# Performance work log

Hardware: AMD Instinct MI355X
Metric: run time of the kernel (lower is better)

## Reference

```python
import jax, jax.numpy as jnp
import numpy as np

N = 50000
E = 800000
DIN = 128
HID = 128
H = 4
C = HID // H  # 32
NEG_SLOPE = 0.2


def _lin(k, fin, fout):
    return jax.random.normal(k, (fin, fout), jnp.float32) * (1.0 / np.sqrt(fin))


def setup_inputs() -> dict:
    key = jax.random.key(0)
    ks = jax.random.split(key, 24)
    x = jax.random.normal(ks[0], (N, DIN), jnp.float32)
    src = jax.random.randint(ks[1], (E,), 0, N)
    dst = (src + jax.random.randint(ks[2], (E,), 1, N)) % N  # no self-loops
    edge_index = jnp.stack([src, dst]).astype(jnp.int32)
    edge_weight = jax.random.uniform(ks[3], (E,), jnp.float32)
    p = {}
    for i, koff in ((0, 4), (1, 12)):
        fin = DIN if i == 0 else HID
        p[f"Wl{i}"] = _lin(ks[koff + 0], fin, HID)
        p[f"bl{i}"] = jnp.zeros((HID,), jnp.float32)
        p[f"Wr{i}"] = _lin(ks[koff + 1], fin, HID)
        p[f"br{i}"] = jnp.zeros((HID,), jnp.float32)
        p[f"We{i}"] = _lin(ks[koff + 2], 1, HID)
        p[f"att{i}"] = jax.random.normal(ks[koff + 3], (H, C), jnp.float32) * (1.0 / np.sqrt(C))
        p[f"b{i}"] = jnp.zeros((HID,), jnp.float32)
    p["prelu_a"] = jnp.float32(0.25)
    return dict(x=x, edge_index=edge_index, edge_weight=edge_weight, **p)


def gatv2_layer(x, src, dst, ea, Wl, bl, Wr, br, We, att, bias):
    n = x.shape[0]
    # self-loop edge_attr = per-dst mean of incoming edge_attr (fill_value='mean')
    deg = jax.ops.segment_sum(jnp.ones((ea.shape[0],), ea.dtype), dst, num_segments=n)
    loop_ea = jax.ops.segment_sum(ea, dst, num_segments=n) / jnp.maximum(deg, 1.0)[:, None]
    loops = jnp.arange(n, dtype=src.dtype)
    srcf = jnp.concatenate([src, loops])
    dstf = jnp.concatenate([dst, loops])
    eaf = jnp.concatenate([ea, loop_ea], axis=0)
    xl = (x @ Wl + bl).reshape(n, H, C)  # source transform (lin_l)
    xr = (x @ Wr + br).reshape(n, H, C)  # target transform (lin_r)
    eproj = (eaf @ We).reshape(-1, H, C)  # lin_edge, bias=False
    m = xl[srcf] + xr[dstf] + eproj  # [E+N, H, C]
    s = jnp.where(m >= 0, m, NEG_SLOPE * m)  # LeakyReLU(0.2)
    logits = jnp.einsum("ehc,hc->eh", s, att)
    # segment softmax over dst
    lmax = jax.lax.stop_gradient(jax.ops.segment_max(logits, dstf, num_segments=n))
    a = jnp.exp(logits - lmax[dstf])
    denom = jax.ops.segment_sum(a, dstf, num_segments=n)
    a = a / denom[dstf]
    out = jax.ops.segment_sum(a[:, :, None] * xl[srcf], dstf, num_segments=n)
    return out.reshape(n, H * C) + bias


def reference(x, edge_index, edge_weight,
              Wl0, bl0, Wr0, br0, We0, att0, b0,
              Wl1, bl1, Wr1, br1, We1, att1, b1,
              prelu_a):
    src, dst = edge_index[0], edge_index[1]
    ea = edge_weight[:, None]  # [E, 1]
    h = gatv2_layer(x, src, dst, ea, Wl0, bl0, Wr0, br0, We0, att0, b0)
    h = jnp.where(h >= 0, h, prelu_a * h)  # PReLU (dropout=0 -> identity)
    h = gatv2_layer(h, src, dst, ea, Wl1, bl1, Wr1, br1, We1, att1, b1)
    return h
```

## Files before the change

kernel.cpp:

```cpp
#include <hip/hip_runtime.h>
#include <hip/hip_bf16.h>
#include <math.h>

#define NN 50000
#define NE 800000
#define HD 128
#define MNEG (-1e30f)
#define LOG2E 1.44269504088896340736f

typedef __attribute__((ext_vector_type(8))) short short8;
typedef __attribute__((ext_vector_type(16))) float f32x16;

__global__ void k_edge_count(const int* __restrict__ ei,
                             int* __restrict__ deg, int* __restrict__ rank) {
    int e = blockIdx.x * blockDim.x + threadIdx.x;
    if (e >= NE) return;
    int d = ei[NE + e];
    rank[e] = atomicAdd(&deg[d], 1);
}

__global__ void k_scan1(const int* __restrict__ deg, int* __restrict__ offs,
                        int* __restrict__ bsums) {
    __shared__ int sh[256];
    int t = threadIdx.x;
    int i = blockIdx.x * 256 + t;
    int v = (i < NN) ? deg[i] : 0;
    sh[t] = v;
    __syncthreads();
    for (int off = 1; off < 256; off <<= 1) {
        int x = (t >= off) ? sh[t - off] : 0;
        __syncthreads();
        sh[t] += x;
        __syncthreads();
    }
    if (i < NN) offs[i] = sh[t] - v;
    if (t == 255) bsums[blockIdx.x] = sh[255];
}

__global__ void k_scan2(int* __restrict__ bsums, int nb) {
    __shared__ int sh[256];
    int t = threadIdx.x;
    int v = (t < nb) ? bsums[t] : 0;
    sh[t] = v;
    __syncthreads();
    for (int off = 1; off < 256; off <<= 1) {
        int x = (t >= off) ? sh[t - off] : 0;
        __syncthreads();
        sh[t] += x;
        __syncthreads();
    }
    if (t < nb) bsums[t] = sh[t] - v;
}

__global__ void k_scan3(int* __restrict__ offs, const int* __restrict__ bsums) {
    int i = blockIdx.x * 256 + threadIdx.x;
    if (i == 0) offs[NN] = NE;
    if (i >= NN) return;
    offs[i] += bsums[blockIdx.x];
}

__global__ void k_csr_fill(const int* __restrict__ ei, const float* __restrict__ ew,
                           const int* __restrict__ rank, const int* __restrict__ offs,
                           int2* __restrict__ csr) {
    int e = blockIdx.x * blockDim.x + threadIdx.x;
    if (e >= NE) return;
    int d = ei[NE + e];
    csr[offs[d] + rank[e]] = make_int2(ei[e], __float_as_int(ew[e]));
}

__device__ __forceinline__ void f2bf2(float x, short& h, short& l) {
    __hip_bfloat16 hb = __float2bfloat16(x);
    float hf = __bfloat162float(hb);
    __hip_bfloat16 lb = __float2bfloat16(x - hf);
    h = *reinterpret_cast<short*>(&hb);
    l = *reinterpret_cast<short*>(&lb);
}

__device__ __forceinline__ void load8(const float* __restrict__ p, float* r) {
    float4 t0 = *(const float4*)p;
    float4 t1 = *(const float4*)(p + 4);
    r[0] = t0.x; r[1] = t0.y; r[2] = t0.z; r[3] = t0.w;
    r[4] = t1.x; r[5] = t1.y; r[6] = t1.z; r[7] = t1.w;
}

__global__ void k_pack(const float* __restrict__ Wl, const float* __restrict__ Wr,
                       short* __restrict__ bhi, short* __restrict__ blo) {
    int idx = blockIdx.x * blockDim.x + threadIdx.x;
    if (idx >= 8 * 8 * 64 * 8) return;
    int j = idx & 7;
    int lane = (idx >> 3) & 63;
    int q = (idx >> 9) & 7;
    int t = idx >> 12;
    int col = t * 32 + (lane & 31);
    int k = q * 16 + ((lane >> 5) << 3) + j;
    float v = (col < 128) ? Wl[k * 128 + col] : Wr[k * 128 + (col - 128)];
    short h, l;
    f2bf2(v, h, l);
    bhi[idx] = h;
    blo[idx] = l;
}

template <bool AF32>
__global__ __launch_bounds__(256, 3) void k_gemm_mfma(
        const float* __restrict__ Af,
        const short* __restrict__ Ahi, const short* __restrict__ Alo,
        const short* __restrict__ Bhi, const short* __restrict__ Blo,
        const float* __restrict__ bl, const float* __restrict__ br,
        float* __restrict__ outl, float* __restrict__ outr) {
    int ch = blockIdx.x & 1;
    int rowblk = blockIdx.x >> 1;
    int lane = threadIdx.x & 63;
    int m0 = rowblk * 128 + (threadIdx.x >> 6) * 32;
    if (m0 >= NN) return;

    int arow = m0 + (lane & 31);
    size_t abase = (size_t)(arow < NN ? arow : 0) * HD + ((lane >> 5) << 3);

    f32x16 acc[4];
#pragma unroll
    for (int t = 0; t < 4; ++t)
#pragma unroll
        for (int r = 0; r < 16; ++r) acc[t][r] = 0.f;

    const short8* Bh8 = (const short8*)Bhi;
    const short8* Bl8 = (const short8*)Blo;

#pragma unroll
    for (int q = 0; q < 8; ++q) {
        short8 ah, al;
        if constexpr (AF32) {
            float vv[8];
            load8(&Af[abase + q * 16], vv);
#pragma unroll
            for (int k2 = 0; k2 < 8; ++k2) {
                short h, l;
                f2bf2(vv[k2], h, l);
                ah[k2] = h;
                al[k2] = l;
            }
        } else {
            ah = *(const short8*)(Ahi + abase + q * 16);
            al = *(const short8*)(Alo + abase + q * 16);
        }
#pragma unroll
        for (int t2 = 0; t2 < 4; ++t2) {
            int t = ch * 4 + t2;
            short8 bh = Bh8[(t * 8 + q) * 64 + lane];
            short8 bl_ = Bl8[(t * 8 + q) * 64 + lane];
            acc[t2] = __builtin_amdgcn_mfma_f32_32x32x16_bf16(ah, bh, acc[t2], 0, 0, 0);
            acc[t2] = __builtin_amdgcn_mfma_f32_32x32x16_bf16(al, bh, acc[t2], 0, 0, 0);
            acc[t2] = __builtin_amdgcn_mfma_f32_32x32x16_bf16(ah, bl_, acc[t2], 0, 0, 0);
        }
    }

    int colr = lane & 31;
    int rowoff = (lane >> 5) << 2;
#pragma unroll
    for (int t2 = 0; t2 < 4; ++t2) {
        int colg = (ch * 4 + t2) * 32 + colr;
        float bias = (colg < 128) ? bl[colg] : br[colg - 128];
        float* dst = (colg < 128) ? (outl + colg) : (outr + (colg - 128));
#pragma unroll
        for (int r = 0; r < 16; ++r) {
            int rw = m0 + (r & 3) + ((r >> 2) << 3) + rowoff;
            if (rw < NN) dst[(size_t)rw * HD] = acc[t2][r] + bias;
        }
    }
}


__device__ __forceinline__ float dotpart(const float* xv, const float* xrv,
                                         const float* wev, const float* atv, float w) {
    float part = 0.f;
#pragma unroll
    for (int k = 0; k < 8; ++k) {
        float t = fmaf(w, wev[k], xrv[k]) + xv[k];
        t = fmaxf(t, 0.2f * t);
        part = fmaf(atv[k], t, part);
    }
    part += __shfl_xor(part, 1);
    part += __shfl_xor(part, 2);
    return part;
}

__device__ __forceinline__ void upd(float part, const float* xv,
                                    float& m, float& s, float* o) {
    float newm = fmaxf(m, part);
    float sc = exp2f(m - newm);
    float p = exp2f(part - newm);
    s = fmaf(s, sc, p);
#pragma unroll
    for (int k = 0; k < 8; ++k) o[k] = fmaf(o[k], sc, p * xv[k]);
    m = newm;
}

template <bool PRELU, bool OUTBF>
__global__ __launch_bounds__(256) void k_node(
        const float* __restrict__ xl, const float* __restrict__ xr,
        const int* __restrict__ offs, const int2* __restrict__ csr,
        const float* __restrict__ We, const float* __restrict__ att,
        const float* __restrict__ bias, const float* __restrict__ prelu,
        float* __restrict__ out, short* __restrict__ ohi, short* __restrict__ olo) {
    int wid = (blockIdx.x * blockDim.x + threadIdx.x) >> 6;
    if (wid >= NN) return;
    const int lane = threadIdx.x & 63;
    const int g = lane >> 4;
    const int j = lane & 15;
    const int c0 = j << 3;
    const int v = wid;

    float xrv[8], wev[8], atv[8];
    load8(&xr[(size_t)v * HD + c0], xrv);
    load8(&We[c0], wev);
    load8(&att[c0], atv);
#pragma unroll
    for (int k = 0; k < 8; ++k) atv[k] *= LOG2E;

    const int beg = offs[v];
    const int deg = offs[v + 1] - beg;

    float mA = MNEG, sA = 0.f, mB = MNEG, sB = 0.f, wsum = 0.f;
    float oA[8], oB[8];
#pragma unroll
    for (int k = 0; k < 8; ++k) { oA[k] = 0.f; oB[k] = 0.f; }

    int i = g;
    for (; i + 4 < deg; i += 8) {
        int2 e0 = csr[beg + i];
        int2 e1 = csr[beg + i + 4];
        float w0 = __int_as_float(e0.y), w1 = __int_as_float(e1.y);
        float xv0[8], xv1[8];
        load8(&xl[(size_t)e0.x * HD + c0], xv0);
        load8(&xl[(size_t)e1.x * HD + c0], xv1);
        float p0 = dotpart(xv0, xrv, wev, atv, w0);
        float p1 = dotpart(xv1, xrv, wev, atv, w1);
        upd(p0, xv0, mA, sA, oA);
        upd(p1, xv1, mB, sB, oB);
        wsum += w0 + w1;
    }
    if (i < deg) {
        int2 e0 = csr[beg + i];
        float w0 = __int_as_float(e0.y);
        float xv0[8];
        load8(&xl[(size_t)e0.x * HD + c0], xv0);
        float p0 = dotpart(xv0, xrv, wev, atv, w0);
        upd(p0, xv0, mA, sA, oA);
        wsum += w0;
    }

    float m, s, o[8];
    {
        m = fmaxf(mA, mB);
        float a = exp2f(mA - m), b = exp2f(mB - m);
        s = sA * a + sB * b;
#pragma unroll
        for (int k = 0; k < 8; ++k) o[k] = oA[k] * a + oB[k] * b;
    }

#pragma unroll
    for (int d = 16; d < 64; d <<= 1) {
        float m2 = __shfl_xor(m, d);
        float s2 = __shfl_xor(s, d);
        wsum += __shfl_xor(wsum, d);
        float M = fmaxf(m, m2);
        float a = exp2f(m - M), b = exp2f(m2 - M);
        s = s * a + s2 * b;
#pragma unroll
        for (int k = 0; k < 8; ++k) {
            float o2 = __shfl_xor(o[k], d);
            o[k] = o[k] * a + o2 * b;
        }
        m = M;
    }

    {
        float wself = wsum / fmaxf((float)deg, 1.f);
        float xv[8];
        load8(&xl[(size_t)v * HD + c0], xv);
        float part = dotpart(xv, xrv, wev, atv, wself);
        float newm = fmaxf(m, part);
        float a = exp2f(m - newm), p = exp2f(part - newm);
        s = s * a + p;
#pragma unroll
        for (int k = 0; k < 8; ++k) o[k] = fmaf(o[k], a, p * xv[k]);
    }

    if (g == 0) {
        float bi[8];
        load8(&bias[c0], bi);
        float inv = 1.f / s;
        float r[8];
#pragma unroll
        for (int k = 0; k < 8; ++k) r[k] = fmaf(o[k], inv, bi[k]);
        if (PRELU) {
            float a = *prelu;
#pragma unroll
            for (int k = 0; k < 8; ++k) r[k] = (r[k] >= 0.f) ? r[k] : a * r[k];
        }
        if (OUTBF) {
            short8 h8, l8;
#pragma unroll
            for (int k = 0; k < 8; ++k) {
                short h, l;
                f2bf2(r[k], h, l);
                h8[k] = h;
                l8[k] = l;
            }
            *(short8*)&ohi[(size_t)v * HD + c0] = h8;
            *(short8*)&olo[(size_t)v * HD + c0] = l8;
        } else {
            float* op = &out[(size_t)v * HD + c0];
            *(float4*)op = make_float4(r[0], r[1], r[2], r[3]);
            *(float4*)(op + 4) = make_float4(r[4], r[5], r[6], r[7]);
        }
    }
}

extern "C" void kernel_launch(void* const* d_in, const int* in_sizes, int n_in,
                              void* d_out, int out_size, void* d_ws, size_t ws_size,
                              hipStream_t stream) {
    const float* x    = (const float*)d_in[0];
    const int*   ei   = (const int*)d_in[1];
    const float* ew   = (const float*)d_in[2];
    const float* Wl0  = (const float*)d_in[3];
    const float* bl0  = (const float*)d_in[4];
    const float* Wr0  = (const float*)d_in[5];
    const float* br0  = (const float*)d_in[6];
    const float* We0  = (const float*)d_in[7];
    const float* att0 = (const float*)d_in[8];
    const float* b0   = (const float*)d_in[9];
    const float* Wl1  = (const float*)d_in[10];
    const float* bl1  = (const float*)d_in[11];
    const float* Wr1  = (const float*)d_in[12];
    const float* br1  = (const float*)d_in[13];
    const float* We1  = (const float*)d_in[14];
    const float* att1 = (const float*)d_in[15];
    const float* b1   = (const float*)d_in[16];
    const float* prelu= (const float*)d_in[17];
    float* out = (float*)d_out;

    char* ws = (char*)d_ws;
    size_t off = 0;
    auto alloc = [&](size_t bytes) {
        char* p = ws + off;
        off += (bytes + 255) & ~size_t(255);
        return p;
    };
    float* bufA   = (float*)alloc(sizeof(float) * NN * HD);
    float* bufB   = (float*)alloc(sizeof(float) * NN * HD);
    short* ahi    = (short*)alloc(sizeof(short) * NN * HD);
    short* alo    = (short*)alloc(sizeof(short) * NN * HD);
    int*   deg    = (int*)alloc(sizeof(int) * NN);
    int*   rank   = (int*)alloc(sizeof(int) * NE);
    int*   offs   = (int*)alloc(sizeof(int) * (NN + 1));
    int*   bsums  = (int*)alloc(sizeof(int) * 256);
    int2*  csr    = (int2*)alloc(sizeof(int2) * NE);
    short* bp0h   = (short*)alloc(sizeof(short) * 32768);
    short* bp0l   = (short*)alloc(sizeof(short) * 32768);
    short* bp1h   = (short*)alloc(sizeof(short) * 32768);
    short* bp1l   = (short*)alloc(sizeof(short) * 32768);
    (void)ws_size; (void)in_sizes; (void)n_in; (void)out_size;

    hipMemsetAsync(deg, 0, sizeof(int) * NN, stream);

    const int EB = (NE + 255) / 256;
    const int NB = (NN + 255) / 256;

    k_edge_count<<<EB, 256, 0, stream>>>(ei, deg, rank);
    k_scan1<<<NB, 256, 0, stream>>>(deg, offs, bsums);
    k_scan2<<<1, 256, 0, stream>>>(bsums, NB);
    k_scan3<<<NB, 256, 0, stream>>>(offs, bsums);
    k_csr_fill<<<EB, 256, 0, stream>>>(ei, ew, rank, offs, csr);

    k_pack<<<128, 256, 0, stream>>>(Wl0, Wr0, bp0h, bp0l);
    k_pack<<<128, 256, 0, stream>>>(Wl1, Wr1, bp1h, bp1l);

    const int GB = 2 * ((NN + 127) / 128);
    const int VB = (NN * 64 + 255) / 256;

    k_gemm_mfma<true><<<GB, 256, 0, stream>>>(x, nullptr, nullptr, bp0h, bp0l,
                                              bl0, br0, bufA, bufB);
    k_node<true, true><<<VB, 256, 0, stream>>>(bufA, bufB, offs, csr,
                                               We0, att0, b0, prelu,
                                               nullptr, ahi, alo);
    k_gemm_mfma<false><<<GB, 256, 0, stream>>>(nullptr, ahi, alo, bp1h, bp1l,
                                               bl1, br1, bufA, bufB);
    k_node<false, false><<<VB, 256, 0, stream>>>(bufA, bufB, offs, csr,
                                                 We1, att1, b1, nullptr,
                                                 out, nullptr, nullptr);
}
```

Before: 367.8 us.

## Stage packed weights in LDS and make GEMM persistent over row blocks

The GEMM kernel now copies its half of the packed bf16 hi/lo weight fragments (64 KB) into shared memory once per block. It then loops persistently over row blocks with a fixed grid of 400 blocks, instead of re-reading weights from global memory for every 128-row tile. Bias loads are hoisted out of the loop, launch bounds drop to 2 blocks per CU to fit the LDS, and the two weight-pack launches are merged into one. The aim is less global/L2 traffic for B; the cost is lower occupancy and fewer blocks in flight to hide A-load latency.

Measured after the change: 348.9 us. -5.1%, faster.

```diff
diff --git a/kernel.cpp b/kernel.cpp
--- a/kernel.cpp
+++ b/kernel.cpp
@@ -83,87 +83,118 @@
     r[4] = t1.x; r[5] = t1.y; r[6] = t1.z; r[7] = t1.w;
 }
 
-__global__ void k_pack(const float* __restrict__ Wl, const float* __restrict__ Wr,
-                       short* __restrict__ bhi, short* __restrict__ blo) {
-    int idx = blockIdx.x * blockDim.x + threadIdx.x;
-    if (idx >= 8 * 8 * 64 * 8) return;
+__global__ void k_pack(const float* __restrict__ Wl0, const float* __restrict__ Wr0,
+                       const float* __restrict__ Wl1, const float* __restrict__ Wr1,
+                       short* __restrict__ b0h, short* __restrict__ b0l,
+                       short* __restrict__ b1h, short* __restrict__ b1l) {
+    int gi = blockIdx.x * blockDim.x + threadIdx.x;
+    if (gi >= 2 * 32768) return;
+    int layer = gi >> 15;
+    int idx = gi & 32767;
     int j = idx & 7;
     int lane = (idx >> 3) & 63;
     int q = (idx >> 9) & 7;
     int t = idx >> 12;
     int col = t * 32 + (lane & 31);
     int k = q * 16 + ((lane >> 5) << 3) + j;
+    const float* Wl = layer ? Wl1 : Wl0;
+    const float* Wr = layer ? Wr1 : Wr0;
     float v = (col < 128) ? Wl[k * 128 + col] : Wr[k * 128 + (col - 128)];
     short h, l;
     f2bf2(v, h, l);
-    bhi[idx] = h;
-    blo[idx] = l;
+    if (layer) { b1h[idx] = h; b1l[idx] = l; }
+    else       { b0h[idx] = h; b0l[idx] = l; }
 }
 
 template <bool AF32>
-__global__ __launch_bounds__(256, 3) void k_gemm_mfma(
+__global__ __launch_bounds__(256, 2) void k_gemm_mfma(
         const float* __restrict__ Af,
         const short* __restrict__ Ahi, const short* __restrict__ Alo,
         const short* __restrict__ Bhi, const short* __restrict__ Blo,
         const float* __restrict__ bl, const float* __restrict__ br,
         float* __restrict__ outl, float* __restrict__ outr) {
-    int ch = blockIdx.x & 1;
-    int rowblk = blockIdx.x >> 1;
-    int lane = threadIdx.x & 63;
-    int m0 = rowblk * 128 + (threadIdx.x >> 6) * 32;
-    if (m0 >= NN) return;
-
-    int arow = m0 + (lane & 31);
-    size_t abase = (size_t)(arow < NN ? arow : 0) * HD + ((lane >> 5) << 3);
-
-    f32x16 acc[4];
-#pragma unroll
-    for (int t = 0; t < 4; ++t)
-#pragma unroll
-        for (int r = 0; r < 16; ++r) acc[t][r] = 0.f;
-
-    const short8* Bh8 = (const short8*)Bhi;
-    const short8* Bl8 = (const short8*)Blo;
-
-#pragma unroll
-    for (int q = 0; q < 8; ++q) {
-        short8 ah, al;
-        if constexpr (AF32) {
-            float vv[8];
-            load8(&Af[abase + q * 16], vv);
-#pragma unroll
-            for (int k2 = 0; k2 < 8; ++k2) {
-                short h, l;
-                f2bf2(vv[k2], h, l);
-                ah[k2] = h;
-                al[k2] = l;
-            }
-        } else {
-            ah = *(const short8*)(Ahi + abase + q * 16);
-            al = *(const short8*)(Alo + abase + q * 16);
-        }
-#pragma unroll
-        for (int t2 = 0; t2 < 4; ++t2) {
-            int t = ch * 4 + t2;
-            short8 bh = Bh8[(t * 8 + q) * 64 + lane];
-            short8 bl_ = Bl8[(t * 8 + q) * 64 + lane];
-            acc[t2] = __builtin_amdgcn_mfma_f32_32x32x16_bf16(ah, bh, acc[t2], 0, 0, 0);
-            acc[t2] = __builtin_amdgcn_mfma_f32_32x32x16_bf16(al, bh, acc[t2], 0, 0, 0);
-            acc[t2] = __builtin_amdgcn_mfma_f32_32x32x16_bf16(ah, bl_, acc[t2], 0, 0, 0);
-        }
-    }
-
-    int colr = lane & 31;
-    int rowoff = (lane >> 5) << 2;
+    __shared__ short ldsh[16384];
+    __shared__ short ldsl[16384];
+    const int ch = blockIdx.x & 1;
+    const int blk = blockIdx.x >> 1;
+    const int nblk = gridDim.x >> 1;
+    const int tid = threadIdx.x;
+    const int lane = tid & 63;
+    const int wid = tid >> 6;
+
+    {
+        const short8* gh = (const short8*)(Bhi + ch * 16384);
+        const short8* gl = (const short8*)(Blo + ch * 16384);
+        short8* lh = (short8*)ldsh;
+        short8* ll = (short8*)ldsl;
+#pragma unroll
+        for (int i = 0; i < 8; ++i) {
+            lh[tid + i * 256] = gh[tid + i * 256];
+            ll[tid + i * 256] = gl[tid + i * 256];
+        }
+    }
+    __syncthreads();
+
+    const int colr = lane & 31;
+    const int rowoff = (lane >> 5) << 2;
+
+    float biasv[4];
 #pragma unroll
     for (int t2 = 0; t2 < 4; ++t2) {
         int colg = (ch * 4 + t2) * 32 + colr;
-        float bias = (colg < 128) ? bl[colg] : br[colg - 128];
-        float* dst = (colg < 128) ? (outl + colg) : (outr + (colg - 128));
-#pragma unroll
-        for (int r = 0; r < 16; ++r) {
-            int rw = m0 + (r & 3) + ((r >> 2) << 3) + rowoff;
-            if (rw < NN) dst[(size_t)rw * HD] = acc[t2][r] + bias;
+        biasv[t2] = (colg < 128) ? bl[colg] : br[colg - 128];
+    }
+
+    for (int m0base = blk * 128; m0base < NN; m0base += nblk * 128) {
+        int m0 = m0base + wid * 32;
+        if (m0 >= NN) continue;
+
+        int arow = m0 + (lane & 31);
+        size_t abase = (size_t)(arow < NN ? arow : 0) * HD + ((lane >> 5) << 3);
+
+        f32x16 acc[4];
+#pragma unroll
+        for (int t2 = 0; t2 < 4; ++t2)
+#pragma unroll
+            for (int r = 0; r < 16; ++r) acc[t2][r] = 0.f;
+
+#pragma unroll
+        for (int q = 0; q < 8; ++q) {
+            short8 ah, al;
+            if constexpr (AF32) {
+                float vv[8];
+                load8(&Af[abase + q * 16], vv);
+#pragma unroll
+                for (int k2 = 0; k2 < 8; ++k2) {
+                    short h, l;
+                    f2bf2(vv[k2], h, l);
+                    ah[k2] = h;
+                    al[k2] = l;
+                }
+            } else {
+                ah = *(const short8*)(Ahi + abase + q * 16);
+                al = *(const short8*)(Alo + abase + q * 16);
+            }
+#pragma unroll
+            for (int t2 = 0; t2 < 4; ++t2) {
+                int fi = ((t2 * 8 + q) * 64 + lane) * 8;
+                short8 bh = *(const short8*)&ldsh[fi];
+                short8 bl_ = *(const short8*)&ldsl[fi];
+                acc[t2] = __builtin_amdgcn_mfma_f32_32x32x16_bf16(ah, bh, acc[t2], 0, 0, 0);
+                acc[t2] = __builtin_amdgcn_mfma_f32_32x32x16_bf16(al, bh, acc[t2], 0, 0, 0);
+                acc[t2] = __builtin_amdgcn_mfma_f32_32x32x16_bf16(ah, bl_, acc[t2], 0, 0, 0);
+            }
+        }
+
+#pragma unroll
+        for (int t2 = 0; t2 < 4; ++t2) {
+            int colg = (ch * 4 + t2) * 32 + colr;
+            float* dst = (colg < 128) ? (outl + colg) : (outr + (colg - 128));
+#pragma unroll
+            for (int r = 0; r < 16; ++r) {
+                int rw = m0 + (r & 3) + ((r >> 2) << 3) + rowoff;
+                if (rw < NN) dst[(size_t)rw * HD] = acc[t2][r] + biasv[t2];
+            }
         }
     }
 }
@@ -372,10 +403,9 @@
     k_scan3<<<NB, 256, 0, stream>>>(offs, bsums);
     k_csr_fill<<<EB, 256, 0, stream>>>(ei, ew, rank, offs, csr);
 
-    k_pack<<<128, 256, 0, stream>>>(Wl0, Wr0, bp0h, bp0l);
-    k_pack<<<128, 256, 0, stream>>>(Wl1, Wr1, bp1h, bp1l);
-
-    const int GB = 2 * ((NN + 127) / 128);
+    k_pack<<<256, 256, 0, stream>>>(Wl0, Wr0, Wl1, Wr1, bp0h, bp0l, bp1h, bp1l);
+
+    const int GB = 2 * 200;
     const int VB = (NN * 64 + 255) / 256;
 
     k_gemm_mfma<true><<<GB, 256, 0, stream>>>(x, nullptr, nullptr, bp0h, bp0l,
```
